# Kernel tuning notes

Hardware: AMD Instinct MI355X
Metric: run time of the kernel (lower is better)

The kernel has to match this reference:

```python
import jax, jax.numpy as jnp
import numpy as np

# --- static mask-construction config (mirrors FlexAttnFunc.init_mask args) ---
B = 1
L_F, L_H, L_W = 8, 20, 36      # latent_shape[2:]
A_F, A_H, A_W = 8, 1, 1        # action_shape[2:]
PATCH = (1, 2, 2)
CHUNK = 1
PAD = 176
WINDOW = 6
DIM, HEADS, DHEAD = 1536, 12, 128
EPS = 1e-5


def _make_ids():
    lf, lh, lw = L_F // PATCH[0], L_H // PATCH[1], L_W // PATCH[2]
    lat_seq = np.repeat(np.arange(B), lf * lh * lw)
    act_seq = np.repeat(np.arange(B), A_F * A_H * A_W)
    seq = np.concatenate([lat_seq, lat_seq, act_seq, act_seq])
    lat_fr = np.broadcast_to(np.arange(L_F)[None, :, None, None], (B, L_F, lh, lw)).reshape(-1)
    act_fr = np.broadcast_to(np.arange(A_F)[None, :, None, None], (B, A_F, A_H, A_W)).reshape(-1)
    fr = np.concatenate([lat_fr // CHUNK * 2] * 2 + [act_fr // CHUNK * 2 + 1] * 2)
    nz = np.concatenate([np.zeros_like(lat_fr), np.ones_like(lat_fr),
                         np.zeros_like(act_fr), np.ones_like(act_fr)])
    pad = np.full(PAD, -1, dtype=np.int64)
    return (np.concatenate([seq, pad]).astype(np.int32),
            np.concatenate([fr, pad]).astype(np.int32),
            np.concatenate([nz, pad]).astype(np.int32))


def setup_inputs() -> dict:
    key = jax.random.key(0)
    ks = jax.random.split(key, 8)
    seq, fr, nz = _make_ids()
    S = seq.shape[0]  # 3072
    sd = 0.02
    return {
        'x': jax.random.normal(ks[0], (1, S, DIM), jnp.float32),
        'Wq': jax.random.normal(ks[1], (DIM, DIM), jnp.float32) * sd,
        'bq': jnp.zeros((DIM,), jnp.float32),
        'Wk': jax.random.normal(ks[2], (DIM, DIM), jnp.float32) * sd,
        'bk': jnp.zeros((DIM,), jnp.float32),
        'Wv': jax.random.normal(ks[3], (DIM, DIM), jnp.float32) * sd,
        'bv': jnp.zeros((DIM,), jnp.float32),
        'gq': 1.0 + jax.random.normal(ks[4], (DIM,), jnp.float32) * sd,
        'gk': 1.0 + jax.random.normal(ks[5], (DIM,), jnp.float32) * sd,
        'Wo': jax.random.normal(ks[6], (DIM, DIM), jnp.float32) * sd,
        'bo': jnp.zeros((DIM,), jnp.float32),
        'seq_ids': jnp.asarray(seq),
        'frame_ids': jnp.asarray(fr),
        'noise_ids': jnp.asarray(nz),
        'window_size': WINDOW,
    }


def _rms(u, g):
    # torch.nn.RMSNorm over last dim (size heads*dim_head), elementwise affine
    return u * jax.lax.rsqrt(jnp.mean(u * u, axis=-1, keepdims=True) + EPS) * g


def _mask(seq_ids, frame_ids, noise_ids, window_size):
    sq, sk = seq_ids[:, None], seq_ids[None, :]
    fq, fk = frame_ids[:, None], frame_ids[None, :]
    nq, nk = noise_ids[:, None], noise_ids[None, :]
    seq_ok = (sq == sk) & (sq >= 0) & (sk >= 0)
    c2c = (nq == 1) & (nk == 1) & (fk <= fq)      # clean->clean, block causal incl self
    n2c = (nq == 0) & (nk == 1) & (fk < fq)       # noise->clean, causal excl self
    n2n = (nq == 0) & (nk == 0) & (fk == fq)      # noise->noise, same frame only
    win = jnp.abs(fq - fk) <= window_size
    return (c2c | n2c | n2n) & seq_ok & win


def reference(x, Wq, bq, Wk, bk, Wv, bv, gq, gk, Wo, bo,
              seq_ids, frame_ids, noise_ids, window_size):
    S = x.shape[1]
    q = _rms(x @ Wq + bq, gq)[0].reshape(S, HEADS, DHEAD)
    k = _rms(x @ Wk + bk, gk)[0].reshape(S, HEADS, DHEAD)
    v = (x @ Wv + bv)[0].reshape(S, HEADS, DHEAD)
    mask = _mask(seq_ids, frame_ids, noise_ids, window_size)  # [S,S] bool
    scores = jnp.einsum('qhd,khd->hqk', q, k) * (DHEAD ** -0.5)
    scores = jnp.where(mask[None], scores, jnp.float32(-1e9))
    attn = jax.nn.softmax(scores, axis=-1)
    o = jnp.einsum('hqk,khd->qhd', attn, v)
    # zero out padded (fully-masked) query rows
    o = o * (seq_ids >= 0).astype(o.dtype)[:, None, None]
    y = o.reshape(1, S, HEADS * DHEAD) @ Wo + bo
    return y
```

## Files before the change

kernel.cpp:

```cpp
#include <hip/hip_runtime.h>
#include <hip/hip_bf16.h>
#include <stdint.h>

typedef __bf16 bf16x8 __attribute__((ext_vector_type(8)));
typedef float f32x4 __attribute__((ext_vector_type(4)));

__device__ __forceinline__ unsigned short f2bf(float f) {
  union { float f; unsigned int u; } v; v.f = f;
  unsigned int u = v.u;
  unsigned int r = (u + 0x7fffu + ((u >> 16) & 1u)) >> 16;
  return (unsigned short)r;
}
__device__ __forceinline__ float bf2f(unsigned short s) {
  union { unsigned int u; float f; } v; v.u = ((unsigned int)s) << 16; return v.f;
}

__global__ __launch_bounds__(256) void conv_f2bf(const float* __restrict__ in,
                                                 unsigned short* __restrict__ out, int n4) {
  int i = blockIdx.x * 256 + threadIdx.x;
  if (i < n4) {
    float4 v = ((const float4*)in)[i];
    ushort4 o;
    o.x = f2bf(v.x); o.y = f2bf(v.y); o.z = f2bf(v.z); o.w = f2bf(v.w);
    ((ushort4*)out)[i] = o;
  }
}

__global__ __launch_bounds__(256) void prep_bitmap(const int* __restrict__ seq,
                                                   const int* __restrict__ fr,
                                                   const int* __restrict__ nz,
                                                   const int* __restrict__ wsz,
                                                   unsigned long long* __restrict__ tbm,
                                                   int S) {
  __shared__ int ks_[3072];
  __shared__ unsigned int tm_[96];
  int tid = threadIdx.x, W = wsz[0];
  for (int i = tid; i < S; i += 256) {
    int sq = seq[i];
    ks_[i] = (sq < 0) ? 0 : ((1 << 9) | ((nz[i] & 1) << 8) | (fr[i] & 15) | (sq << 10));
  }
  __syncthreads();
  for (int t = tid; t < S / 32; t += 256) {
    unsigned int m = 0;
    for (int j = 0; j < 32; j++) {
      int a = ks_[t * 32 + j];
      if (a & (1 << 9)) m |= (a & (1 << 8)) ? (1u << (16 + (a & 15))) : (1u << (a & 15));
    }
    tm_[t] = m;
  }
  __syncthreads();
  for (int qg = tid; qg < S / 16; qg += 256) {
    unsigned int allowed = 0;
    for (int j = 0; j < 16; j++) {
      int a = ks_[qg * 16 + j];
      if (!(a & (1 << 9))) continue;
      int fq = a & 15, nq = (a >> 8) & 1;
      int lo = fq - W; if (lo < 0) lo = 0;
      unsigned int lom = ~((1u << lo) - 1);
      if (nq) allowed |= (((1u << (fq + 1)) - 1) & lom) << 16;
      else    allowed |= ((((1u << fq) - 1) & lom) << 16) | (1u << fq);
    }
    unsigned long long b0 = 0, b1 = 0;
    for (int t = 0; t < 96; t++)
      if (tm_[t] & allowed) { if (t < 64) b0 |= 1ull << t; else b1 |= 1ull << (t - 64); }
    tbm[qg * 2] = b0; tbm[qg * 2 + 1] = b1;
  }
}

__global__ __launch_bounds__(256) void prep_mask(const int* __restrict__ seq,
                                                 const int* __restrict__ fr,
                                                 const int* __restrict__ nz,
                                                 const int* __restrict__ wsz,
                                                 unsigned char* __restrict__ mb, int S) {
  int qg = blockIdx.y, t0 = blockIdx.x * 4;
  __shared__ int qs[16], qf_[16], qn[16], ksq[128], kfr[128], knz[128];
  int tid = threadIdx.x;
  if (tid < 16) {
    int q = qg * 16 + tid; qs[tid] = seq[q]; qf_[tid] = fr[q]; qn[tid] = nz[q];
  } else if (tid < 144) {
    int i = tid - 16; int k = t0 * 32 + i;
    ksq[i] = seq[k]; kfr[i] = fr[k]; knz[i] = nz[k];
  }
  __syncthreads();
  int wave = tid >> 6, lane = tid & 63, quad = lane >> 4, l16 = lane & 15;
  int W = wsz[0];
  unsigned int byte = 0;
  for (int nt = 0; nt < 2; nt++)
    for (int r = 0; r < 4; r++) {
      int qi = quad * 4 + r;
      int ki = wave * 32 + nt * 16 + l16;
      bool ok  = (qs[qi] == ksq[ki]) && (qs[qi] >= 0) && (ksq[ki] >= 0);
      bool c2c = (qn[qi] == 1) && (knz[ki] == 1) && (kfr[ki] <= qf_[qi]);
      bool n2c = (qn[qi] == 0) && (knz[ki] == 1) && (kfr[ki] <  qf_[qi]);
      bool n2n = (qn[qi] == 0) && (knz[ki] == 0) && (kfr[ki] == qf_[qi]);
      int df = qf_[qi] - kfr[ki]; df = df < 0 ? -df : df;
      if ((c2c || n2c || n2n) && ok && (df <= W)) byte |= 1u << (nt * 4 + r);
    }
  mb[((size_t)qg * 96 + t0 + wave) * 64 + lane] = (unsigned char)byte;
}

__global__ __launch_bounds__(256) void conv_wt4(const float* __restrict__ W0,
                                                const float* __restrict__ W1,
                                                const float* __restrict__ W2,
                                                const float* __restrict__ W3,
                                                unsigned short* __restrict__ Wt) {
  const int K = 1536, N = 1536;
  const float* W = blockIdx.z == 0 ? W0 : (blockIdx.z == 1 ? W1 : (blockIdx.z == 2 ? W2 : W3));
  __shared__ __align__(16) unsigned short t[64][65];
  int k0 = blockIdx.x * 64, n0 = blockIdx.y * 64;
  for (int i = 0; i < 16; i++) {
    int e = threadIdx.x + i * 256;
    int r = e >> 6, c = e & 63;
    t[r][c] = f2bf(W[(size_t)(k0 + r) * N + n0 + c]);
  }
  __syncthreads();
  for (int i = 0; i < 16; i++) {
    int e = threadIdx.x + i * 256;
    int r = e >> 6, c = e & 63;
    Wt[(size_t)(blockIdx.z * 1536 + n0 + r) * K + k0 + c] = t[c][r];
  }
}

__global__ __launch_bounds__(256) void gemm_qkv(
    const unsigned short* __restrict__ A, const unsigned short* __restrict__ Bt,
    const float* __restrict__ bq, const float* __restrict__ bk, const float* __restrict__ bv,
    unsigned short* __restrict__ qt, unsigned short* __restrict__ ktb,
    unsigned short* __restrict__ vtb, float* __restrict__ ssq, int S) {
  const int K = 1536;
  __shared__ __align__(16) unsigned short smem[16384];
  unsigned short* As = smem;
  unsigned short* Bs = smem + 8192;
  unsigned short* Cs = smem;
  int tid = threadIdx.x, wave = tid >> 6, lane = tid & 63;
  int quad = lane >> 4, l16 = lane & 15;
  int m0 = blockIdx.x * 128, n0 = blockIdx.y * 128;
  int wm = (wave & 1) * 64, wn = (wave >> 1) * 64;
  int lr = lane >> 3, lc = (lane & 7) * 8;
  f32x4 acc[4][4] = {};
  for (int k0 = 0; k0 < K; k0 += 64) {
    for (int c = 0; c < 4; c++) {
      int chunk = wave * 4 + c;
      int row = chunk * 8 + lr;
      const unsigned short* ga = &A[(size_t)(m0 + row) * K + k0 + lc];
      const unsigned short* gb = &Bt[(size_t)(n0 + row) * K + k0 + lc];
      __builtin_amdgcn_global_load_lds(
          (const __attribute__((address_space(1))) unsigned int*)ga,
          (__attribute__((address_space(3))) unsigned int*)(As + chunk * 512), 16, 0, 0);
      __builtin_amdgcn_global_load_lds(
          (const __attribute__((address_space(1))) unsigned int*)gb,
          (__attribute__((address_space(3))) unsigned int*)(Bs + chunk * 512), 16, 0, 0);
    }
    __syncthreads();
    for (int kk = 0; kk < 64; kk += 32) {
      bf16x8 af[4], bfr[4];
      for (int i = 0; i < 4; i++)
        af[i] = *(const bf16x8*)&As[(wm + i * 16 + l16) * 64 + kk + quad * 8];
      for (int j = 0; j < 4; j++)
        bfr[j] = *(const bf16x8*)&Bs[(wn + j * 16 + l16) * 64 + kk + quad * 8];
      for (int i = 0; i < 4; i++)
        for (int j = 0; j < 4; j++)
          acc[i][j] = __builtin_amdgcn_mfma_f32_16x16x32_bf16(af[i], bfr[j], acc[i][j], 0, 0, 0);
    }
    __syncthreads();
  }
  int region = (n0 >= 3072) ? 2 : (n0 >= 1536 ? 1 : 0);
  int cbase = n0 - region * 1536;
  int hh = cbase >> 7;
  if (region < 2) {
    const float* bias = region == 0 ? bq : bk;
    float* ssqp = ssq + region * 3072;
    float ss[4][4] = {};
    for (int j = 0; j < 4; j++) {
      int col = cbase + wn + j * 16 + l16;
      float b = bias[col];
      int cp = wn + j * 16 + l16;
      for (int i = 0; i < 4; i++)
        for (int r = 0; r < 4; r++) {
          float v = acc[i][j][r] + b;
          ss[i][r] += v * v;
          int sp = wm + i * 16 + quad * 4 + r;
          Cs[sp * 128 + cp] = f2bf(v);
        }
    }
    for (int i = 0; i < 4; i++)
      for (int r = 0; r < 4; r++) {
        float v = ss[i][r];
        for (int o = 1; o < 16; o <<= 1) v += __shfl_xor(v, o);
        if (l16 == 0)
          atomicAdd(&ssqp[m0 + wm + i * 16 + quad * 4 + r], v);
      }
    __syncthreads();
    unsigned short* outp = (region == 0 ? qt : ktb) + (size_t)hh * 393216 + (size_t)m0 * 128;
    for (int p = 0; p < 8; p++) {
      int o = p * 2048 + tid * 8;
      *(uint4*)&outp[o] = *(const uint4*)&Cs[o];
    }
  } else {
    for (int j = 0; j < 4; j++) {
      int d = cbase + wn + j * 16 + l16;
      float b = bv[d];
      int cp = wn + j * 16 + l16;
      int c8 = l16 * 8;
      for (int i = 0; i < 4; i++)
        for (int r = 0; r < 4; r++) {
          int sp = wm + i * 16 + quad * 4 + r;
          Cs[cp * 128 + (sp ^ c8)] = f2bf(acc[i][j][r] + b);
        }
    }
    __syncthreads();
    unsigned short* outp = vtb + ((size_t)hh * 96 + (m0 >> 5)) * 4096;
    for (int p = 0; p < 8; p++) {
      int o = p * 2048 + tid * 8;
      int tile = o >> 12, rem = o & 4095;
      int dd = rem >> 5, s31 = rem & 31;
      int laddr = dd * 128 + ((tile * 32 + s31) ^ ((dd & 15) * 8));
      *(uint4*)&outp[o] = *(const uint4*)&Cs[laddr];
    }
  }
}

__global__ __launch_bounds__(192) void rms_scale(unsigned short* __restrict__ qt,
                                                 unsigned short* __restrict__ ktb,
                                                 const float* __restrict__ ssq,
                                                 const float* __restrict__ gq,
                                                 const float* __restrict__ gk) {
  int row = blockIdx.x, buf = blockIdx.y;
  unsigned short* p = buf ? ktb : qt;
  const float* g = buf ? gk : gq;
  float sc = rsqrtf(ssq[buf * 3072 + row] * (1.0f / 1536.0f) + 1e-5f);
  int c = threadIdx.x * 8;
  int hh = c >> 7, dd = c & 127;
  size_t idx = (size_t)hh * 393216 + (size_t)row * 128 + dd;
  ushort4 a = *(ushort4*)&p[idx];
  ushort4 b = *(ushort4*)&p[idx + 4];
  float4 g0 = *(const float4*)&g[c];
  float4 g1 = *(const float4*)&g[c + 4];
  a.x = f2bf(bf2f(a.x) * sc * g0.x); a.y = f2bf(bf2f(a.y) * sc * g0.y);
  a.z = f2bf(bf2f(a.z) * sc * g0.z); a.w = f2bf(bf2f(a.w) * sc * g0.w);
  b.x = f2bf(bf2f(b.x) * sc * g1.x); b.y = f2bf(bf2f(b.y) * sc * g1.y);
  b.z = f2bf(bf2f(b.z) * sc * g1.z); b.w = f2bf(bf2f(b.w) * sc * g1.w);
  *(ushort4*)&p[idx] = a;
  *(ushort4*)&p[idx + 4] = b;
}

__global__ __launch_bounds__(256) void gemm_wo(
    const unsigned short* __restrict__ A, const unsigned short* __restrict__ Bt,
    const float* __restrict__ bias, float* __restrict__ C, int M, int N, int K) {
  __shared__ __align__(16) unsigned short As[128 * 64];
  __shared__ __align__(16) unsigned short Bs[64 * 64];
  int tid = threadIdx.x, wave = tid >> 6, lane = tid & 63;
  int quad = lane >> 4, l16 = lane & 15;
  int m0 = blockIdx.x * 128, n0 = blockIdx.y * 64;
  int wm = (wave & 1) * 64, wn = (wave >> 1) * 32;
  int lr = lane >> 3, lc = (lane & 7) * 8;
  f32x4 acc[4][2] = {};
  for (int k0 = 0; k0 < K; k0 += 64) {
    for (int c = 0; c < 4; c++) {
      int chunk = wave * 4 + c;
      int row = chunk * 8 + lr;
      const unsigned short* ga = &A[(size_t)(m0 + row) * K + k0 + lc];
      __builtin_amdgcn_global_load_lds(
          (const __attribute__((address_space(1))) unsigned int*)ga,
          (__attribute__((address_space(3))) unsigned int*)(As + chunk * 512), 16, 0, 0);
    }
    for (int c = 0; c < 2; c++) {
      int chunk = wave * 2 + c;
      int row = chunk * 8 + lr;
      const unsigned short* gb = &Bt[(size_t)(n0 + row) * K + k0 + lc];
      __builtin_amdgcn_global_load_lds(
          (const __attribute__((address_space(1))) unsigned int*)gb,
          (__attribute__((address_space(3))) unsigned int*)(Bs + chunk * 512), 16, 0, 0);
    }
    __syncthreads();
    for (int kk = 0; kk < 64; kk += 32) {
      bf16x8 af[4], bfr[2];
      for (int i = 0; i < 4; i++)
        af[i] = *(const bf16x8*)&As[(wm + i * 16 + l16) * 64 + kk + quad * 8];
      for (int j = 0; j < 2; j++)
        bfr[j] = *(const bf16x8*)&Bs[(wn + j * 16 + l16) * 64 + kk + quad * 8];
      for (int i = 0; i < 4; i++)
        for (int j = 0; j < 2; j++)
          acc[i][j] = __builtin_amdgcn_mfma_f32_16x16x32_bf16(af[i], bfr[j], acc[i][j], 0, 0, 0);
    }
    __syncthreads();
  }
  for (int j = 0; j < 2; j++) {
    int col = n0 + wn + j * 16 + l16;
    float b = bias[col];
    for (int i = 0; i < 4; i++)
      for (int r = 0; r < 4; r++)
        C[(size_t)(m0 + wm + i * 16 + quad * 4 + r) * N + col] = acc[i][j][r] + b;
  }
}

__global__ __launch_bounds__(256) void attn(
    const unsigned short* __restrict__ qt,
    const unsigned short* __restrict__ kt,
    const unsigned short* __restrict__ vt,
    const unsigned char* __restrict__ mb,
    const unsigned long long* __restrict__ tbm,
    unsigned short* __restrict__ op0b, unsigned short* __restrict__ op1b,
    float* __restrict__ lp, int S) {
  const int h = blockIdx.x;
  const int qb64 = blockIdx.y;
  const int split = blockIdx.z;
  int tid = threadIdx.x, wave = tid >> 6, lane = tid & 63;
  int quad = lane >> 4, l16 = lane & 15;
  const float scale = 0.088388347648318447f;

  __shared__ __align__(16) unsigned short Ks[2][4096];
  __shared__ __align__(16) unsigned short Vs[2][4096];
  __shared__ __align__(16) unsigned short pshare[4][16][40];

  int qg = qb64 * 4 + wave;
  unsigned long long bm0 = tbm[(qb64 * 4) * 2]     | tbm[(qb64 * 4 + 1) * 2] |
                           tbm[(qb64 * 4 + 2) * 2] | tbm[(qb64 * 4 + 3) * 2];
  unsigned long long bm1 = tbm[(qb64 * 4) * 2 + 1]     | tbm[(qb64 * 4 + 1) * 2 + 1] |
                           tbm[(qb64 * 4 + 2) * 2 + 1] | tbm[(qb64 * 4 + 3) * 2 + 1];
  unsigned long long wb0 = tbm[qg * 2], wb1 = tbm[qg * 2 + 1];

  const unsigned short* kth = kt + (size_t)h * 96 * 4096;
  const unsigned short* vth = vt + (size_t)h * 96 * 4096;
  const unsigned char* mbq = mb + (size_t)qg * 96 * 64;

  bf16x8 qf[4];
  {
    const unsigned short* qp = qt + ((size_t)(h * 192 + qg) * 16 + l16) * 128 + quad * 8;
    for (int ks = 0; ks < 4; ks++) qf[ks] = *(const bf16x8*)&qp[ks * 32];
  }

  f32x4 oacc[8] = {};
  f32x4 lacc = {};
  const __bf16 onebf = (__bf16)1.0f;
  const bf16x8 ones = {onebf, onebf, onebf, onebf, onebf, onebf, onebf, onebf};

#define POP(dst) do { \
    if (bm0) { dst = __builtin_ctzll(bm0); bm0 &= bm0 - 1; } \
    else if (bm1) { dst = 64 + __builtin_ctzll(bm1); bm1 &= bm1 - 1; } \
    else dst = -1; } while (0)

#define STAGE(t_, b_) do { \
    for (int j = 0; j < 2; j++) { \
      int slot = j * 256 + tid; \
      int key = slot >> 4, cc = slot & 15; \
      const unsigned short* src = kth + (size_t)(t_) * 4096 + key * 128 + (cc ^ (key & 15)) * 8; \
      __builtin_amdgcn_global_load_lds( \
          (const __attribute__((address_space(1))) unsigned int*)src, \
          (__attribute__((address_space(3))) unsigned int*)(&Ks[b_][0] + j * 2048 + wave * 512), \
          16, 0, 0); \
    } \
    for (int j = 0; j < 2; j++) { \
      int slot = j * 256 + tid; \
      int row = slot >> 2, cc = slot & 3; \
      const unsigned short* src = vth + (size_t)(t_) * 4096 + row * 32 + (cc ^ ((row >> 1) & 3)) * 8; \
      __builtin_amdgcn_global_load_lds( \
          (const __attribute__((address_space(1))) unsigned int*)src, \
          (__attribute__((address_space(3))) unsigned int*)(&Vs[b_][0] + j * 2048 + wave * 512), \
          16, 0, 0); \
    } } while (0)

  int t, dsc;
  if (split) POP(dsc);
  POP(t);
  unsigned int mbyte = 0;
  if (t >= 0) { STAGE(t, 0); mbyte = mbq[t * 64 + lane]; }
  __syncthreads();
  int buf = 0;

  while (t >= 0) {
    POP(dsc);
    int tn; POP(tn);
    unsigned int mbyte2 = 0;
    if (tn >= 0) { STAGE(tn, buf ^ 1); mbyte2 = mbq[tn * 64 + lane]; }

    bool live = (t < 64) ? ((wb0 >> t) & 1) : ((wb1 >> (t - 64)) & 1);
    if (live) {
      f32x4 sacc[2] = {};
      for (int nt = 0; nt < 2; nt++) {
        int key = nt * 16 + l16;
        for (int ks = 0; ks < 4; ks++) {
          int cc = (ks * 4 + quad) ^ l16;
          bf16x8 kf = *(const bf16x8*)&Ks[buf][(key * 16 + cc) * 8];
          sacc[nt] = __builtin_amdgcn_mfma_f32_16x16x32_bf16(qf[ks], kf, sacc[nt], 0, 0, 0);
        }
      }
      for (int nt = 0; nt < 2; nt++)
        for (int r = 0; r < 4; r++) {
          float e = __expf(sacc[nt][r] * scale - 16.0f);
          float p = ((mbyte >> (nt * 4 + r)) & 1) ? e : 0.0f;
          pshare[wave][quad * 4 + r][nt * 16 + l16] = f2bf(p);
        }
      __asm__ __volatile__("s_waitcnt lgkmcnt(0)" ::: "memory");
      bf16x8 pf = *(const bf16x8*)&pshare[wave][l16][quad * 8];
      for (int d = 0; d < 8; d++) {
        int row = d * 16 + l16;
        int cc = quad ^ ((l16 >> 1) & 3);
        bf16x8 vf = *(const bf16x8*)&Vs[buf][(row * 4 + cc) * 8];
        oacc[d] = __builtin_amdgcn_mfma_f32_16x16x32_bf16(pf, vf, oacc[d], 0, 0, 0);
      }
      lacc = __builtin_amdgcn_mfma_f32_16x16x32_bf16(pf, ones, lacc, 0, 0, 0);
    }
    __syncthreads();
    buf ^= 1;
    t = tn;
    mbyte = mbyte2;
  }
#undef POP
#undef STAGE

  unsigned short* po = split ? op1b : op0b;
  for (int r = 0; r < 4; r++) {
    int q = qb64 * 64 + wave * 16 + quad * 4 + r;
    float inv = (lacc[r] > 0.f) ? 1.0f / lacc[r] : 0.0f;
    for (int d = 0; d < 8; d++)
      po[((size_t)h * S + q) * 128 + d * 16 + l16] = f2bf(oacc[d][r] * inv);
    if (l16 == 0)
      lp[((size_t)split * 12 + h) * S + q] = lacc[r];
  }
}

__global__ __launch_bounds__(256) void combine(const unsigned short* __restrict__ op0b,
                                               const unsigned short* __restrict__ op1b,
                                               const float* __restrict__ lp,
                                               const int* __restrict__ seq,
                                               unsigned short* __restrict__ ob, int S) {
  int e4 = blockIdx.x * 256 + threadIdx.x;
  int idx = e4 * 4;
  int per_h = S * 128;
  int h = idx / per_h;
  int rem = idx - h * per_h;
  int q = rem >> 7, dd = rem & 127;
  float l0 = lp[(size_t)h * S + q], l1 = lp[(size_t)(12 + h) * S + q];
  float tot = l0 + l1;
  float ok = (seq[q] >= 0 && tot > 0.f) ? 1.0f / tot : 0.0f;
  float w0 = l0 * ok, w1 = l1 * ok;
  ushort4 a = ((const ushort4*)op0b)[e4];
  ushort4 b = ((const ushort4*)op1b)[e4];
  ushort4 o;
  o.x = f2bf(bf2f(a.x) * w0 + bf2f(b.x) * w1);
  o.y = f2bf(bf2f(a.y) * w0 + bf2f(b.y) * w1);
  o.z = f2bf(bf2f(a.z) * w0 + bf2f(b.z) * w1);
  o.w = f2bf(bf2f(a.w) * w0 + bf2f(b.w) * w1);
  *(ushort4*)&ob[(size_t)q * 1536 + h * 128 + dd] = o;
}

extern "C" void kernel_launch(void* const* d_in, const int* in_sizes, int n_in,
                              void* d_out, int out_size, void* d_ws, size_t ws_size,
                              hipStream_t stream) {
  const float* x  = (const float*)d_in[0];
  const float* Wq = (const float*)d_in[1];
  const float* bq = (const float*)d_in[2];
  const float* Wk = (const float*)d_in[3];
  const float* bk = (const float*)d_in[4];
  const float* Wv = (const float*)d_in[5];
  const float* bv = (const float*)d_in[6];
  const float* gq = (const float*)d_in[7];
  const float* gk = (const float*)d_in[8];
  const float* Wo = (const float*)d_in[9];
  const float* bo = (const float*)d_in[10];
  const int* seq  = (const int*)d_in[11];
  const int* fr   = (const int*)d_in[12];
  const int* nz   = (const int*)d_in[13];
  const int* wsz  = (const int*)d_in[14];
  float* out = (float*)d_out;
  const int S = in_sizes[11];
  const int D = 1536;

  char* ws = (char*)d_ws;
  size_t off = 0;
  unsigned short* x_bf = (unsigned short*)(ws + off); off += (size_t)S * D * 2;
  unsigned short* wt   = (unsigned short*)(ws + off); off += (size_t)4 * D * D * 2;
  unsigned short* qt   = (unsigned short*)(ws + off); off += (size_t)S * D * 2;
  unsigned short* ktb  = (unsigned short*)(ws + off); off += (size_t)S * D * 2;
  unsigned short* vtb  = (unsigned short*)(ws + off); off += (size_t)S * D * 2;
  unsigned short* o_bf = (unsigned short*)(ws + off); off += (size_t)S * D * 2;
  unsigned short* op0b = (unsigned short*)(ws + off); off += (size_t)S * D * 2;
  unsigned short* op1b = (unsigned short*)(ws + off); off += (size_t)S * D * 2;
  unsigned long long* tbm = (unsigned long long*)(ws + off); off += (size_t)(S / 16) * 16;
  unsigned char*  mbuf = (unsigned char*)(ws + off);  off += (size_t)(S / 16) * 96 * 64;
  float*          lp   = (float*)(ws + off);          off += (size_t)2 * 12 * S * 4;
  float*          ssq  = (float*)(ws + off);          off += (size_t)2 * 3072 * 4;

  dim3 blk(256);
  conv_f2bf<<<dim3((S * D / 4 + 255) / 256), blk, 0, stream>>>(x, x_bf, S * D / 4);
  prep_bitmap<<<dim3(1), blk, 0, stream>>>(seq, fr, nz, wsz, tbm, S);
  prep_mask<<<dim3(24, S / 16), blk, 0, stream>>>(seq, fr, nz, wsz, mbuf, S);
  conv_wt4<<<dim3(D / 64, D / 64, 4), blk, 0, stream>>>(Wq, Wk, Wv, Wo, wt);
  hipMemsetAsync(ssq, 0, (size_t)2 * 3072 * 4, stream);
  gemm_qkv<<<dim3(S / 128, 3 * D / 128), blk, 0, stream>>>(x_bf, wt, bq, bk, bv,
                                                           qt, ktb, vtb, ssq, S);
  rms_scale<<<dim3(S, 2), dim3(192), 0, stream>>>(qt, ktb, ssq, gq, gk);
  attn<<<dim3(D / 128, S / 64, 2), blk, 0, stream>>>(qt, ktb, vtb, mbuf, tbm,
                                                     op0b, op1b, lp, S);
  combine<<<dim3(12 * S * 128 / 4 / 256), blk, 0, stream>>>(op0b, op1b, lp, seq, o_bf, S);
  gemm_wo<<<dim3(S / 128, D / 64), blk, 0, stream>>>(o_bf, wt + (size_t)3 * D * D,
                                                     bo, out, S, D, D);
}
```

Measured before the change: 325.3 us.

## Merge prep kernels into one setup launch and fold RMS scaling into attention

Combines the x conversion, weight transpose/convert, bitmap, mask prep and ssq memset into a single multi-role setup kernel, cutting several launches. Drops the separate rms_scale pass: gq*gk is folded into the K columns in the QKV GEMM epilogue, and the per-row q/k rsqrt norms are applied to the scores inside attention. This removes a read-modify-write pass over Q and K. In exchange the attention inner loop does extra rsqrt and loads per tile, and numerics shift slightly because normalization now happens after bf16 rounding of the unnormalized values.

After: 310.8 us. 1.05x faster.

```diff
diff --git a/kernel.cpp b/kernel.cpp
--- a/kernel.cpp
+++ b/kernel.cpp
@@ -15,115 +15,118 @@
   union { unsigned int u; float f; } v; v.u = ((unsigned int)s) << 16; return v.f;
 }
 
-__global__ __launch_bounds__(256) void conv_f2bf(const float* __restrict__ in,
-                                                 unsigned short* __restrict__ out, int n4) {
-  int i = blockIdx.x * 256 + threadIdx.x;
-  if (i < n4) {
-    float4 v = ((const float4*)in)[i];
-    ushort4 o;
-    o.x = f2bf(v.x); o.y = f2bf(v.y); o.z = f2bf(v.z); o.w = f2bf(v.w);
-    ((ushort4*)out)[i] = o;
-  }
-}
-
-__global__ __launch_bounds__(256) void prep_bitmap(const int* __restrict__ seq,
-                                                   const int* __restrict__ fr,
-                                                   const int* __restrict__ nz,
-                                                   const int* __restrict__ wsz,
-                                                   unsigned long long* __restrict__ tbm,
-                                                   int S) {
-  __shared__ int ks_[3072];
-  __shared__ unsigned int tm_[96];
-  int tid = threadIdx.x, W = wsz[0];
-  for (int i = tid; i < S; i += 256) {
-    int sq = seq[i];
-    ks_[i] = (sq < 0) ? 0 : ((1 << 9) | ((nz[i] & 1) << 8) | (fr[i] & 15) | (sq << 10));
-  }
-  __syncthreads();
-  for (int t = tid; t < S / 32; t += 256) {
-    unsigned int m = 0;
-    for (int j = 0; j < 32; j++) {
-      int a = ks_[t * 32 + j];
-      if (a & (1 << 9)) m |= (a & (1 << 8)) ? (1u << (16 + (a & 15))) : (1u << (a & 15));
-    }
-    tm_[t] = m;
-  }
-  __syncthreads();
-  for (int qg = tid; qg < S / 16; qg += 256) {
-    unsigned int allowed = 0;
-    for (int j = 0; j < 16; j++) {
-      int a = ks_[qg * 16 + j];
-      if (!(a & (1 << 9))) continue;
-      int fq = a & 15, nq = (a >> 8) & 1;
-      int lo = fq - W; if (lo < 0) lo = 0;
-      unsigned int lom = ~((1u << lo) - 1);
-      if (nq) allowed |= (((1u << (fq + 1)) - 1) & lom) << 16;
-      else    allowed |= ((((1u << fq) - 1) & lom) << 16) | (1u << fq);
-    }
-    unsigned long long b0 = 0, b1 = 0;
-    for (int t = 0; t < 96; t++)
-      if (tm_[t] & allowed) { if (t < 64) b0 |= 1ull << t; else b1 |= 1ull << (t - 64); }
-    tbm[qg * 2] = b0; tbm[qg * 2 + 1] = b1;
-  }
-}
-
-__global__ __launch_bounds__(256) void prep_mask(const int* __restrict__ seq,
-                                                 const int* __restrict__ fr,
-                                                 const int* __restrict__ nz,
-                                                 const int* __restrict__ wsz,
-                                                 unsigned char* __restrict__ mb, int S) {
-  int qg = blockIdx.y, t0 = blockIdx.x * 4;
-  __shared__ int qs[16], qf_[16], qn[16], ksq[128], kfr[128], knz[128];
-  int tid = threadIdx.x;
-  if (tid < 16) {
-    int q = qg * 16 + tid; qs[tid] = seq[q]; qf_[tid] = fr[q]; qn[tid] = nz[q];
-  } else if (tid < 144) {
-    int i = tid - 16; int k = t0 * 32 + i;
-    ksq[i] = seq[k]; kfr[i] = fr[k]; knz[i] = nz[k];
-  }
-  __syncthreads();
-  int wave = tid >> 6, lane = tid & 63, quad = lane >> 4, l16 = lane & 15;
-  int W = wsz[0];
-  unsigned int byte = 0;
-  for (int nt = 0; nt < 2; nt++)
-    for (int r = 0; r < 4; r++) {
-      int qi = quad * 4 + r;
-      int ki = wave * 32 + nt * 16 + l16;
-      bool ok  = (qs[qi] == ksq[ki]) && (qs[qi] >= 0) && (ksq[ki] >= 0);
-      bool c2c = (qn[qi] == 1) && (knz[ki] == 1) && (kfr[ki] <= qf_[qi]);
-      bool n2c = (qn[qi] == 0) && (knz[ki] == 1) && (kfr[ki] <  qf_[qi]);
-      bool n2n = (qn[qi] == 0) && (knz[ki] == 0) && (kfr[ki] == qf_[qi]);
-      int df = qf_[qi] - kfr[ki]; df = df < 0 ? -df : df;
-      if ((c2c || n2c || n2n) && ok && (df <= W)) byte |= 1u << (nt * 4 + r);
-    }
-  mb[((size_t)qg * 96 + t0 + wave) * 64 + lane] = (unsigned char)byte;
-}
-
-__global__ __launch_bounds__(256) void conv_wt4(const float* __restrict__ W0,
-                                                const float* __restrict__ W1,
-                                                const float* __restrict__ W2,
-                                                const float* __restrict__ W3,
-                                                unsigned short* __restrict__ Wt) {
-  const int K = 1536, N = 1536;
-  const float* W = blockIdx.z == 0 ? W0 : (blockIdx.z == 1 ? W1 : (blockIdx.z == 2 ? W2 : W3));
-  __shared__ __align__(16) unsigned short t[64][65];
-  int k0 = blockIdx.x * 64, n0 = blockIdx.y * 64;
-  for (int i = 0; i < 16; i++) {
-    int e = threadIdx.x + i * 256;
-    int r = e >> 6, c = e & 63;
-    t[r][c] = f2bf(W[(size_t)(k0 + r) * N + n0 + c]);
-  }
-  __syncthreads();
-  for (int i = 0; i < 16; i++) {
-    int e = threadIdx.x + i * 256;
-    int r = e >> 6, c = e & 63;
-    Wt[(size_t)(blockIdx.z * 1536 + n0 + r) * K + k0 + c] = t[c][r];
+__global__ __launch_bounds__(256) void setup(
+    const float* __restrict__ x,
+    const float* __restrict__ Wq, const float* __restrict__ Wk,
+    const float* __restrict__ Wv, const float* __restrict__ Wo,
+    const int* __restrict__ seq, const int* __restrict__ fr,
+    const int* __restrict__ nz, const int* __restrict__ wsz,
+    unsigned short* __restrict__ x_bf, unsigned short* __restrict__ wt,
+    unsigned long long* __restrict__ tbm, unsigned char* __restrict__ mb,
+    float* __restrict__ ssq, int S) {
+  __shared__ __align__(16) unsigned char smu[16384];
+  int b = blockIdx.x, tid = threadIdx.x;
+  if (b < 1152) {
+    int base = b * 1024 + tid;
+    for (int j = 0; j < 4; j++) {
+      int i = base + j * 256;
+      float4 v = ((const float4*)x)[i];
+      ushort4 o;
+      o.x = f2bf(v.x); o.y = f2bf(v.y); o.z = f2bf(v.z); o.w = f2bf(v.w);
+      ((ushort4*)x_bf)[i] = o;
+    }
+  } else if (b < 3456) {
+    int id = b - 1152;
+    int z = id / 576, rem = id % 576;
+    int kx = rem % 24, ny = rem / 24;
+    const float* W = z == 0 ? Wq : (z == 1 ? Wk : (z == 2 ? Wv : Wo));
+    unsigned short (*t)[65] = (unsigned short(*)[65])smu;
+    int k0 = kx * 64, n0 = ny * 64;
+    const int N = 1536, K = 1536;
+    for (int i = 0; i < 16; i++) {
+      int e = tid + i * 256;
+      int r = e >> 6, c = e & 63;
+      t[r][c] = f2bf(W[(size_t)(k0 + r) * N + n0 + c]);
+    }
+    __syncthreads();
+    for (int i = 0; i < 16; i++) {
+      int e = tid + i * 256;
+      int r = e >> 6, c = e & 63;
+      wt[(size_t)(z * 1536 + n0 + r) * K + k0 + c] = t[c][r];
+    }
+  } else if (b == 3456) {
+    int* ks_ = (int*)smu;
+    unsigned int* tm_ = (unsigned int*)(smu + 12288);
+    int W = wsz[0];
+    for (int i = tid; i < S; i += 256) {
+      int sq = seq[i];
+      ks_[i] = (sq < 0) ? 0 : ((1 << 9) | ((nz[i] & 1) << 8) | (fr[i] & 15) | (sq << 10));
+    }
+    for (int i = tid; i < 6144; i += 256) ssq[i] = 0.f;
+    __syncthreads();
+    for (int t = tid; t < S / 32; t += 256) {
+      unsigned int m = 0;
+      for (int j = 0; j < 32; j++) {
+        int a = ks_[t * 32 + j];
+        if (a & (1 << 9)) m |= (a & (1 << 8)) ? (1u << (16 + (a & 15))) : (1u << (a & 15));
+      }
+      tm_[t] = m;
+    }
+    __syncthreads();
+    for (int qg = tid; qg < S / 16; qg += 256) {
+      unsigned int allowed = 0;
+      for (int j = 0; j < 16; j++) {
+        int a = ks_[qg * 16 + j];
+        if (!(a & (1 << 9))) continue;
+        int fq = a & 15, nq = (a >> 8) & 1;
+        int lo = fq - W; if (lo < 0) lo = 0;
+        unsigned int lom = ~((1u << lo) - 1);
+        if (nq) allowed |= (((1u << (fq + 1)) - 1) & lom) << 16;
+        else    allowed |= ((((1u << fq) - 1) & lom) << 16) | (1u << fq);
+      }
+      unsigned long long b0 = 0, b1 = 0;
+      for (int t = 0; t < 96; t++)
+        if (tm_[t] & allowed) { if (t < 64) b0 |= 1ull << t; else b1 |= 1ull << (t - 64); }
+      tbm[qg * 2] = b0; tbm[qg * 2 + 1] = b1;
+    }
+  } else {
+    int qg = b - 3457;
+    int* ks_ = (int*)smu;
+    int W = wsz[0];
+    for (int i = tid; i < S; i += 256) {
+      int sq = seq[i];
+      ks_[i] = (sq < 0) ? 0 : ((1 << 9) | ((nz[i] & 1) << 8) | (fr[i] & 15) | (sq << 10));
+    }
+    __syncthreads();
+    int wave = tid >> 6, lane = tid & 63, quad = lane >> 4, l16 = lane & 15;
+    int aq[4];
+    for (int r = 0; r < 4; r++) aq[r] = ks_[qg * 16 + quad * 4 + r];
+    for (int t = wave; t < 96; t += 4) {
+      int ak[2] = { ks_[t * 32 + l16], ks_[t * 32 + 16 + l16] };
+      unsigned int byte = 0;
+      for (int nt = 0; nt < 2; nt++) {
+        int a = ak[nt];
+        int kfr = a & 15, knz = (a >> 8) & 1, kvb = (a >> 9) & 1, ksq = a >> 10;
+        for (int r = 0; r < 4; r++) {
+          int bq_ = aq[r];
+          int qfr = bq_ & 15, qnz = (bq_ >> 8) & 1, qvb = (bq_ >> 9) & 1, qsq = bq_ >> 10;
+          bool ok  = qvb && kvb && (qsq == ksq);
+          bool c2c = qnz && knz && (kfr <= qfr);
+          bool n2c = !qnz && knz && (kfr < qfr);
+          bool n2n = !qnz && !knz && (kfr == qfr);
+          int df = qfr - kfr; df = df < 0 ? -df : df;
+          if ((c2c || n2c || n2n) && ok && (df <= W)) byte |= 1u << (nt * 4 + r);
+        }
+      }
+      mb[((size_t)qg * 96 + t) * 64 + lane] = (unsigned char)byte;
+    }
   }
 }
 
 __global__ __launch_bounds__(256) void gemm_qkv(
     const unsigned short* __restrict__ A, const unsigned short* __restrict__ Bt,
     const float* __restrict__ bq, const float* __restrict__ bk, const float* __restrict__ bv,
+    const float* __restrict__ gq, const float* __restrict__ gk,
     unsigned short* __restrict__ qt, unsigned short* __restrict__ ktb,
     unsigned short* __restrict__ vtb, float* __restrict__ ssq, int S) {
   const int K = 1536;
@@ -173,13 +176,13 @@
     for (int j = 0; j < 4; j++) {
       int col = cbase + wn + j * 16 + l16;
       float b = bias[col];
+      float G = (region == 1) ? gq[col] * gk[col] : 1.0f;
       int cp = wn + j * 16 + l16;
       for (int i = 0; i < 4; i++)
         for (int r = 0; r < 4; r++) {
           float v = acc[i][j][r] + b;
           ss[i][r] += v * v;
-          int sp = wm + i * 16 + quad * 4 + r;
-          Cs[sp * 128 + cp] = f2bf(v);
+          Cs[(wm + i * 16 + quad * 4 + r) * 128 + cp] = f2bf(v * G);
         }
     }
     for (int i = 0; i < 4; i++)
@@ -217,30 +220,6 @@
       *(uint4*)&outp[o] = *(const uint4*)&Cs[laddr];
     }
   }
-}
-
-__global__ __launch_bounds__(192) void rms_scale(unsigned short* __restrict__ qt,
-                                                 unsigned short* __restrict__ ktb,
-                                                 const float* __restrict__ ssq,
-                                                 const float* __restrict__ gq,
-                                                 const float* __restrict__ gk) {
-  int row = blockIdx.x, buf = blockIdx.y;
-  unsigned short* p = buf ? ktb : qt;
-  const float* g = buf ? gk : gq;
-  float sc = rsqrtf(ssq[buf * 3072 + row] * (1.0f / 1536.0f) + 1e-5f);
-  int c = threadIdx.x * 8;
-  int hh = c >> 7, dd = c & 127;
-  size_t idx = (size_t)hh * 393216 + (size_t)row * 128 + dd;
-  ushort4 a = *(ushort4*)&p[idx];
-  ushort4 b = *(ushort4*)&p[idx + 4];
-  float4 g0 = *(const float4*)&g[c];
-  float4 g1 = *(const float4*)&g[c + 4];
-  a.x = f2bf(bf2f(a.x) * sc * g0.x); a.y = f2bf(bf2f(a.y) * sc * g0.y);
-  a.z = f2bf(bf2f(a.z) * sc * g0.z); a.w = f2bf(bf2f(a.w) * sc * g0.w);
-  b.x = f2bf(bf2f(b.x) * sc * g1.x); b.y = f2bf(bf2f(b.y) * sc * g1.y);
-  b.z = f2bf(bf2f(b.z) * sc * g1.z); b.w = f2bf(bf2f(b.w) * sc * g1.w);
-  *(ushort4*)&p[idx] = a;
-  *(ushort4*)&p[idx + 4] = b;
 }
 
 __global__ __launch_bounds__(256) void gemm_wo(
@@ -299,6 +278,7 @@
     const unsigned short* __restrict__ vt,
     const unsigned char* __restrict__ mb,
     const unsigned long long* __restrict__ tbm,
+    const float* __restrict__ ssq,
     unsigned short* __restrict__ op0b, unsigned short* __restrict__ op1b,
     float* __restrict__ lp, int S) {
   const int h = blockIdx.x;
@@ -328,6 +308,12 @@
     const unsigned short* qp = qt + ((size_t)(h * 192 + qg) * 16 + l16) * 128 + quad * 8;
     for (int ks = 0; ks < 4; ks++) qf[ks] = *(const bf16x8*)&qp[ks * 32];
   }
+  float qs[4];
+  for (int r = 0; r < 4; r++) {
+    int row = qb64 * 64 + wave * 16 + quad * 4 + r;
+    qs[r] = rsqrtf(ssq[row] * (1.0f / 1536.0f) + 1e-5f) * scale;
+  }
+  const float* ssk = ssq + 3072;
 
   f32x4 oacc[8] = {};
   f32x4 lacc = {};
@@ -363,7 +349,12 @@
   if (split) POP(dsc);
   POP(t);
   unsigned int mbyte = 0;
-  if (t >= 0) { STAGE(t, 0); mbyte = mbq[t * 64 + lane]; }
+  float kss0 = 0.f, kss1 = 0.f;
+  if (t >= 0) {
+    STAGE(t, 0);
+    mbyte = mbq[t * 64 + lane];
+    kss0 = ssk[t * 32 + l16]; kss1 = ssk[t * 32 + 16 + l16];
+  }
   __syncthreads();
   int buf = 0;
 
@@ -371,7 +362,12 @@
     POP(dsc);
     int tn; POP(tn);
     unsigned int mbyte2 = 0;
-    if (tn >= 0) { STAGE(tn, buf ^ 1); mbyte2 = mbq[tn * 64 + lane]; }
+    float nss0 = 0.f, nss1 = 0.f;
+    if (tn >= 0) {
+      STAGE(tn, buf ^ 1);
+      mbyte2 = mbq[tn * 64 + lane];
+      nss0 = ssk[tn * 32 + l16]; nss1 = ssk[tn * 32 + 16 + l16];
+    }
 
     bool live = (t < 64) ? ((wb0 >> t) & 1) : ((wb1 >> (t - 64)) & 1);
     if (live) {
@@ -384,9 +380,12 @@
           sacc[nt] = __builtin_amdgcn_mfma_f32_16x16x32_bf16(qf[ks], kf, sacc[nt], 0, 0, 0);
         }
       }
+      float ksc[2];
+      ksc[0] = rsqrtf(kss0 * (1.0f / 1536.0f) + 1e-5f);
+      ksc[1] = rsqrtf(kss1 * (1.0f / 1536.0f) + 1e-5f);
       for (int nt = 0; nt < 2; nt++)
         for (int r = 0; r < 4; r++) {
-          float e = __expf(sacc[nt][r] * scale - 16.0f);
+          float e = __expf(sacc[nt][r] * (qs[r] * ksc[nt]) - 16.0f);
           float p = ((mbyte >> (nt * 4 + r)) & 1) ? e : 0.0f;
           pshare[wave][quad * 4 + r][nt * 16 + l16] = f2bf(p);
         }
@@ -404,6 +403,7 @@
     buf ^= 1;
     t = tn;
     mbyte = mbyte2;
+    kss0 = nss0; kss1 = nss1;
   }
 #undef POP
 #undef STAGE
@@ -482,15 +482,11 @@
   float*          ssq  = (float*)(ws + off);          off += (size_t)2 * 3072 * 4;
 
   dim3 blk(256);
-  conv_f2bf<<<dim3((S * D / 4 + 255) / 256), blk, 0, stream>>>(x, x_bf, S * D / 4);
-  prep_bitmap<<<dim3(1), blk, 0, stream>>>(seq, fr, nz, wsz, tbm, S);
-  prep_mask<<<dim3(24, S / 16), blk, 0, stream>>>(seq, fr, nz, wsz, mbuf, S);
-  conv_wt4<<<dim3(D / 64, D / 64, 4), blk, 0, stream>>>(Wq, Wk, Wv, Wo, wt);
-  hipMemsetAsync(ssq, 0, (size_t)2 * 3072 * 4, stream);
-  gemm_qkv<<<dim3(S / 128, 3 * D / 128), blk, 0, stream>>>(x_bf, wt, bq, bk, bv,
+  setup<<<dim3(3649), blk, 0, stream>>>(x, Wq, Wk, Wv, Wo, seq, fr, nz, wsz,
+                                        x_bf, wt, tbm, mbuf, ssq, S);
+  gemm_qkv<<<dim3(S / 128, 3 * D / 128), blk, 0, stream>>>(x_bf, wt, bq, bk, bv, gq, gk,
                                                            qt, ktb, vtb, ssq, S);
-  rms_scale<<<dim3(S, 2), dim3(192), 0, stream>>>(qt, ktb, ssq, gq, gk);
-  attn<<<dim3(D / 128, S / 64, 2), blk, 0, stream>>>(qt, ktb, vtb, mbuf, tbm,
+  attn<<<dim3(D / 128, S / 64, 2), blk, 0, stream>>>(qt, ktb, vtb, mbuf, tbm, ssq,
                                                      op0b, op1b, lp, S);
   combine<<<dim3(12 * S * 128 / 4 / 256), blk, 0, stream>>>(op0b, op1b, lp, seq, o_bf, S);
   gemm_wo<<<dim3(S / 128, D / 64), blk, 0, stream>>>(o_bf, wt + (size_t)3 * D * D,
```
